# Kernel tuning notes

Hardware: AMD Instinct MI355X
Metric: run time of the kernel (lower is better)

The kernel has to match this reference:

```python
import jax, jax.numpy as jnp
import numpy as np

B, T, D, H, O = 64, 2048, 1024, 1024, 1024


def setup_inputs() -> dict:
    key = jax.random.key(0)
    ks = jax.random.split(key, 7)
    std = 1.0 / np.sqrt(H)
    u = lambda k, shape: jax.random.uniform(k, shape, jnp.float32, -std, std)
    return {
        "x": jax.random.normal(ks[0], (B, T, D), jnp.float32),
        "Wx": u(ks[1], (3 * H, D)),
        "bx": u(ks[2], (3 * H,)),
        "Wh": u(ks[3], (3 * H, H)),
        "bh": u(ks[4], (3 * H,)),
        "Wf": u(ks[5], (O, H)),
        "bf": u(ks[6], (O,)),
    }


def _gru_forward(x, Wx, bx, Wh, bh, Wf, bf):
    # Precompute input projections for all timesteps: [B, T, 3H]
    x_proj = jnp.einsum('btd,gd->btg', x, Wx) + bx

    def step(h, xp_t):
        # xp_t: [B, 3H], h: [B, H]
        h_proj = h @ Wh.T + bh
        x_r, x_u, x_n = jnp.split(xp_t, 3, axis=1)
        h_r, h_u, h_n = jnp.split(h_proj, 3, axis=1)
        reset = jax.nn.sigmoid(x_r + h_r)
        update = jax.nn.sigmoid(x_u + h_u)
        new = jnp.tanh(x_n + reset * h_n)
        hy = update * h + (1.0 - update) * new
        return hy, None

    h0 = jnp.zeros((x.shape[0], Wh.shape[1]), x.dtype)
    h_last, _ = jax.lax.scan(step, h0, jnp.swapaxes(x_proj, 0, 1))
    logits = h_last @ Wf.T + bf
    return jax.nn.log_softmax(logits, axis=-1)


def reference(x, Wx, bx, Wh, bh, Wf, bf):
    return _gru_forward(x, Wx, bx, Wh, bh, Wf, bf)
```

## Files before the change

kernel.cpp:

```cpp
#include <hip/hip_runtime.h>
#include <hip/hip_bf16.h>


#define Bb 64
#define Tt 2048
#define Dd 1024
#define Hh 1024

typedef __attribute__((ext_vector_type(8))) short bf16x8;
typedef __attribute__((ext_vector_type(4))) float f32x4;
typedef __attribute__((ext_vector_type(4))) unsigned int u32x4;

__device__ __forceinline__ short f2bf(float x) {
    __hip_bfloat16 h = __float2bfloat16(x);
    return __builtin_bit_cast(short, h);
}
__device__ __forceinline__ float bf2f(unsigned short u) {
    return __builtin_bit_cast(float, (unsigned)u << 16);
}
__device__ __forceinline__ bf16x8 pack8(float4 a, float4 b) {
    bf16x8 f;
    f[0] = f2bf(a.x); f[1] = f2bf(a.y); f[2] = f2bf(a.z); f[3] = f2bf(a.w);
    f[4] = f2bf(b.x); f[5] = f2bf(b.y); f[6] = f2bf(b.z); f[7] = f2bf(b.w);
    return f;
}
__device__ __forceinline__ unsigned long long ald64(const void* p) {
    return __hip_atomic_load((const unsigned long long*)p, __ATOMIC_RELAXED,
                             __HIP_MEMORY_SCOPE_AGENT);
}
__device__ __forceinline__ unsigned aldu32(const unsigned* p) {
    return __hip_atomic_load(p, __ATOMIC_RELAXED, __HIP_MEMORY_SCOPE_AGENT);
}

__global__ void wcvt(const float* __restrict__ a, unsigned short* __restrict__ o, long n) {
    long i = ((long)blockIdx.x * blockDim.x + threadIdx.x) * 8;
    long stride = (long)gridDim.x * blockDim.x * 8;
    for (; i < n; i += stride)
        *(bf16x8*)(o + i) = pack8(*(const float4*)(a + i), *(const float4*)(a + i + 4));
}

__global__ __launch_bounds__(256)
void xp_gemm(const float* __restrict__ x, const unsigned short* __restrict__ Wxb,
             unsigned short* __restrict__ xp, int t0) {
    __shared__ unsigned short As[64][40];
    const int tid = threadIdx.x;
    const int wave = tid >> 6, l = tid & 63, lm = l & 15, lk = l >> 4;
    const int slot = blockIdx.y;
    const int t = t0 + slot;
    const int n0w = blockIdx.x * 128 + wave * 32;

    f32x4 acc[4][2] = {};
#pragma unroll 1
    for (int k0 = 0; k0 < 1024; k0 += 32) {
        __syncthreads();
        {
            const int r = tid >> 2, kq = (tid & 3) * 8;
            const float* p = x + (size_t)r * Tt * Dd + (size_t)t * Dd + k0 + kq;
            *(bf16x8*)&As[r][kq] = pack8(*(const float4*)p, *(const float4*)(p + 4));
        }
        __syncthreads();
        bf16x8 bfr[2];
#pragma unroll
        for (int nt = 0; nt < 2; ++nt)
            bfr[nt] = *(const bf16x8*)(Wxb + (size_t)(n0w + nt * 16 + lm) * 1024 + k0 + lk * 8);
#pragma unroll
        for (int mt = 0; mt < 4; ++mt) {
            const bf16x8 af = *(const bf16x8*)&As[mt * 16 + lm][lk * 8];
            acc[mt][0] = __builtin_amdgcn_mfma_f32_16x16x32_bf16(af, bfr[0], acc[mt][0], 0, 0, 0);
            acc[mt][1] = __builtin_amdgcn_mfma_f32_16x16x32_bf16(af, bfr[1], acc[mt][1], 0, 0, 0);
        }
    }
#pragma unroll
    for (int mt = 0; mt < 4; ++mt)
#pragma unroll
        for (int nt = 0; nt < 2; ++nt)
#pragma unroll
            for (int i = 0; i < 4; ++i) {
                const int b = mt * 16 + lk * 4 + i;
                const int n = n0w + nt * 16 + lm;
                xp[((size_t)slot * 64 + b) * 3072 + n] = (unsigned short)f2bf(acc[mt][nt][i]);
            }
}

__global__ __launch_bounds__(512, 2)
void gru_scan8(const float* __restrict__ Wh, const float* __restrict__ bx,
               const float* __restrict__ bh, unsigned short* __restrict__ hl2,
               unsigned short* __restrict__ hmall,
               float* __restrict__ hstate, float* __restrict__ hfinal,
               const unsigned short* __restrict__ xp, unsigned* __restrict__ reg,
               int t0, int tend) {
    const int tid = threadIdx.x;
    const int w = tid >> 6, l = tid & 63, lm = l & 15, lk = l >> 4;

    __shared__ float comb[8][32][100];
    __shared__ float bxv[96], bhv[96];
    __shared__ unsigned s_gc;

    if (tid == 0) {
        unsigned xcc;
        asm volatile("s_getreg_b32 %0, hwreg(HW_REG_XCC_ID)" : "=s"(xcc));
        xcc &= 7u;
        unsigned r = __hip_atomic_fetch_add(&reg[xcc], 1u, __ATOMIC_RELAXED,
                                            __HIP_MEMORY_SCOPE_AGENT);
        __hip_atomic_fetch_add(&reg[8], 1u, __ATOMIC_RELEASE, __HIP_MEMORY_SCOPE_AGENT);
        while (__hip_atomic_load(&reg[8], __ATOMIC_ACQUIRE, __HIP_MEMORY_SCOPE_AGENT) < 256u)
            __builtin_amdgcn_s_sleep(8);
        bool bal = (r < 32u);
        for (int i = 0; i < 8; ++i)
            bal = bal && (__hip_atomic_load(&reg[i], __ATOMIC_RELAXED,
                                            __HIP_MEMORY_SCOPE_AGENT) == 32u);
        const unsigned g = bal ? xcc : (blockIdx.x & 7u);
        const unsigned c = bal ? r : (blockIdx.x >> 3);
        s_gc = (g << 8) | c;
    }
    __syncthreads();
    const int g = (s_gc >> 8) & 7, c = s_gc & 255;
    const int bg0 = g * 8, j0 = c * 32;
    const int kb = w * 128;

    if (tid < 96) {
        const int g3 = tid >> 5, jj = tid & 31;
        bxv[tid] = bx[g3 * 1024 + j0 + jj];
        bhv[tid] = bh[g3 * 1024 + j0 + jj];
    }
    const int grow = tid >> 4, jp = (tid & 15) * 2;
    float hp0 = 0.f, hp1 = 0.f;
    if (tid < 128) {
        const float2 h2 = *(const float2*)(hstate + (size_t)(bg0 + grow) * 1024 + j0 + jp);
        hp0 = h2.x; hp1 = h2.y;
    }

    bf16x8 wf[6][4];
#pragma unroll
    for (int nt = 0; nt < 6; ++nt) {
        const int n96 = nt * 16 + lm, g3 = n96 >> 5, jj = n96 & 31;
        const float* rp = Wh + (size_t)(g3 * 1024 + j0 + jj) * 1024 + kb + lk * 8;
#pragma unroll
        for (int ks = 0; ks < 4; ++ks)
            wf[nt][ks] = pack8(*(const float4*)(rp + ks * 32), *(const float4*)(rp + ks * 32 + 4));
    }
    __syncthreads();

    unsigned xa0 = 0, xa1 = 0, xa2 = 0, xb0 = 0, xb1 = 0, xb2 = 0;
    if (tid < 128) {
        const unsigned short* xr = xp + ((size_t)0 * 64 + bg0 + grow) * 3072 + j0 + jp;
        xa0 = *(const unsigned*)(xr);
        xa1 = *(const unsigned*)(xr + 1024);
        xa2 = *(const unsigned*)(xr + 2048);
    }

    const int row_a = (lm < 8) ? lm : 7;
    u32x4 f0, f1, f2, f3;
    int useMall = 0;

#define L2LOAD4(P)                                                             \
    asm volatile(                                                              \
        "global_load_dwordx4 %[r0], %[ad], off sc0\n\t"                        \
        "global_load_dwordx4 %[r1], %[ad], off offset:64 sc0\n\t"              \
        "global_load_dwordx4 %[r2], %[ad], off offset:128 sc0\n\t"             \
        "global_load_dwordx4 %[r3], %[ad], off offset:192 sc0\n\t"             \
        "s_waitcnt vmcnt(0)"                                                   \
        : [r0] "=&v"(f0), [r1] "=&v"(f1), [r2] "=&v"(f2), [r3] "=&v"(f3)       \
        : [ad] "v"(P)                                                          \
        : "memory")
#define MLOAD4(P)                                                              \
    do {                                                                       \
        struct UU { unsigned long long a, b; };                                \
        UU u0{ald64(P), ald64((P) + 4)};                                       \
        UU u1{ald64((P) + 32), ald64((P) + 36)};                               \
        UU u2{ald64((P) + 64), ald64((P) + 68)};                               \
        UU u3{ald64((P) + 96), ald64((P) + 100)};                              \
        f0 = __builtin_bit_cast(u32x4, u0);                                    \
        f1 = __builtin_bit_cast(u32x4, u1);                                    \
        f2 = __builtin_bit_cast(u32x4, u2);                                    \
        f3 = __builtin_bit_cast(u32x4, u3);                                    \
    } while (0)
#define TAG4(F) (((F)[0] ^ tg) | ((F)[1] ^ tg) | ((F)[2] ^ tg) | ((F)[3] ^ tg))

#pragma unroll 1
    for (int t = t0; t < tend; ++t) {
        const size_t hoff = (size_t)(t & 1) * 65536 + (size_t)g * 8192
                            + (size_t)row_a * 1024 + kb + lk * 8;
        const unsigned tg = (unsigned)(t >> 1) & 1u;

        if (!useMall) {
            const unsigned short* pl = hl2 + hoff;
            int spins = 0;
            for (;;) {
                L2LOAD4(pl);
                const unsigned bad = (TAG4(f0) | TAG4(f1) | TAG4(f2) | TAG4(f3)) & 1u;
                if (__builtin_expect(__all((int)(bad == 0u)), 1)) break;
                if (++spins > 512) { useMall = 1; break; }
            }
        }
        if (useMall) {
            const unsigned short* pm = hmall + hoff;
            for (;;) {
                MLOAD4(pm);
                const unsigned bad = (TAG4(f0) | TAG4(f1) | TAG4(f2) | TAG4(f3)) & 1u;
                if (__builtin_expect(__all((int)(bad == 0u)), 1)) break;
                __builtin_amdgcn_s_sleep(1);
            }
        }

        if (tid < 128 && t + 1 < tend) {
            const unsigned short* xr = xp + ((size_t)(t + 1 - t0) * 64 + bg0 + grow) * 3072 + j0 + jp;
            xb0 = *(const unsigned*)(xr);
            xb1 = *(const unsigned*)(xr + 1024);
            xb2 = *(const unsigned*)(xr + 2048);
        }

        f32x4 acc[6] = {};
#define KSTEP(F, KS)                                                            \
        do {                                                                    \
            const bf16x8 af = __builtin_bit_cast(bf16x8, F);                    \
            _Pragma("unroll")                                                   \
            for (int nt = 0; nt < 6; ++nt)                                      \
                acc[nt] = __builtin_amdgcn_mfma_f32_16x16x32_bf16(              \
                    af, wf[nt][KS], acc[nt], 0, 0, 0);                          \
        } while (0)
        KSTEP(f0, 0); KSTEP(f1, 1); KSTEP(f2, 2); KSTEP(f3, 3);
#undef KSTEP

        if (lk < 2) {
#pragma unroll
            for (int nt = 0; nt < 6; ++nt)
#pragma unroll
                for (int i = 0; i < 4; ++i)
                    comb[w][lk * 4 + i][nt * 16 + lm] = acc[nt][i];
        }
        asm volatile("s_waitcnt lgkmcnt(0)\ns_barrier" ::: "memory");

        if (tid < 128) {
            float s00 = 0, s10 = 0, s20 = 0, s01 = 0, s11 = 0, s21 = 0;
#pragma unroll
            for (int ww = 0; ww < 8; ++ww) {
                s00 += comb[ww][grow][jp];      s01 += comb[ww][grow][jp + 1];
                s10 += comb[ww][grow][32 + jp]; s11 += comb[ww][grow][33 + jp];
                s20 += comb[ww][grow][64 + jp]; s21 += comb[ww][grow][65 + jp];
            }
            const float xr0 = bf2f((unsigned short)xa0) + bxv[jp];
            const float xr1 = bf2f((unsigned short)(xa0 >> 16)) + bxv[jp + 1];
            const float xu0 = bf2f((unsigned short)xa1) + bxv[32 + jp];
            const float xu1 = bf2f((unsigned short)(xa1 >> 16)) + bxv[33 + jp];
            const float xn0 = bf2f((unsigned short)xa2) + bxv[64 + jp];
            const float xn1 = bf2f((unsigned short)(xa2 >> 16)) + bxv[65 + jp];
            const float r0 = 1.0f / (1.0f + __expf(-(xr0 + s00 + bhv[jp])));
            const float r1 = 1.0f / (1.0f + __expf(-(xr1 + s01 + bhv[jp + 1])));
            const float u0 = 1.0f / (1.0f + __expf(-(xu0 + s10 + bhv[32 + jp])));
            const float u1 = 1.0f / (1.0f + __expf(-(xu1 + s11 + bhv[33 + jp])));
            const float z0 = xn0 + r0 * (s20 + bhv[64 + jp]);
            const float z1 = xn1 + r1 * (s21 + bhv[65 + jp]);
            const float e0 = __expf(2.0f * z0), e1 = __expf(2.0f * z1);
            const float n0 = 1.0f - 2.0f / (e0 + 1.0f);
            const float n1 = 1.0f - 2.0f / (e1 + 1.0f);
            const float hy0 = u0 * hp0 + (1.0f - u0) * n0;
            const float hy1 = u1 * hp1 + (1.0f - u1) * n1;
            hp0 = hy0; hp1 = hy1;
            const unsigned tagn = ((unsigned)(t + 1) >> 1) & 1u;
            const unsigned v0 = ((unsigned)(unsigned short)f2bf(hy0) & 0xFFFEu) | tagn;
            const unsigned pk = ((unsigned)(unsigned short)f2bf(hy1) << 16) | v0;
            const size_t soff = (size_t)((t + 1) & 1) * 65536 + (size_t)g * 8192
                                + (size_t)grow * 1024 + j0 + jp;
            *(volatile unsigned*)(hl2 + soff) = pk;
            __hip_atomic_store((unsigned*)(hmall + soff), pk, __ATOMIC_RELAXED,
                               __HIP_MEMORY_SCOPE_AGENT);
            if (t == tend - 1)
                *(float2*)(hstate + (size_t)(bg0 + grow) * 1024 + j0 + jp) = make_float2(hy0, hy1);
            if (t == Tt - 1)
                *(float2*)(hfinal + (size_t)(bg0 + grow) * 1024 + j0 + jp) = make_float2(hy0, hy1);
            xa0 = xb0; xa1 = xb1; xa2 = xb2;
        }
        asm volatile("s_barrier" ::: "memory");
    }
#undef L2LOAD4
#undef MLOAD4
#undef TAG4
}

template <bool RING>
__global__ __launch_bounds__(256, 1)
void gru_scan(const float* __restrict__ x,
              const float* __restrict__ Wx, const float* __restrict__ bx,
              const float* __restrict__ Wh, const float* __restrict__ bh,
              unsigned short* __restrict__ hbuf, float* __restrict__ hfinal,
              unsigned short* __restrict__ ring, unsigned* __restrict__ flags) {
    const int tid = threadIdx.x;
    const int w   = tid >> 6;
    const int l   = tid & 63;
    const int bid = blockIdx.x;
    const int g   = bid & 1;
    const int c   = bid >> 1;
    const int bg0 = g * 32;
    const int j0  = c * 8;

    __shared__ float comb[4][32][24];
    __shared__ float hp[32][8];
    __shared__ float bxv[24], bhv[24];

    hp[tid >> 3][tid & 7] = 0.0f;
    if (tid < 24) {
        const int gate = tid >> 3, jj = tid & 7;
        bxv[tid] = bx[gate * 1024 + j0 + jj];
        bhv[tid] = bh[gate * 1024 + j0 + jj];
    }

    const int lm = l & 15;
    const int lk = l >> 4;
    const int wb = w * 512;
    bf16x8 bfr[2][16];
    {
        const float* Wbase = (w < 2) ? Wx : Wh;
        const int krel = (w < 2) ? wb : (wb - 1024);
#pragma unroll
        for (int nt = 0; nt < 2; ++nt) {
            int row24 = nt * 16 + lm;
            if (row24 > 23) row24 = 23;
            const int gate = row24 >> 3, jj = row24 & 7;
            const float* rp = Wbase + (size_t)(gate * 1024 + j0 + jj) * 1024 + krel + lk * 8;
#pragma unroll
            for (int ks = 0; ks < 16; ++ks) {
                float4 a = *(const float4*)(rp + ks * 32);
                float4 b = *(const float4*)(rp + ks * 32 + 4);
                bfr[nt][ks] = pack8(a, b);
            }
        }
    }
    __syncthreads();

    if (RING) {
        if (tid < 128) {
            const int e = c * 256 + tid * 2;
            const int rl = e >> 10, col = e & 1023;
#pragma unroll
            for (int s = 0; s < 4; ++s) {
                const float2 xv = *(const float2*)(x + ((size_t)(bg0 + rl) * Tt + s) * Dd + col);
                unsigned pk = (unsigned)(unsigned short)f2bf(xv.x)
                            | ((unsigned)(unsigned short)f2bf(xv.y) << 16);
                __hip_atomic_store((unsigned*)(ring + (size_t)s * 65536
                                               + (size_t)(bg0 + rl) * 1024 + col),
                                   pk, __ATOMIC_RELAXED, __HIP_MEMORY_SCOPE_AGENT);
            }
        }
        asm volatile("s_waitcnt vmcnt(0)" ::: "memory");
        __syncthreads();
        if (tid == 0)
            __hip_atomic_store(&flags[g * 128 + c], 1u, __ATOMIC_RELAXED,
                               __HIP_MEMORY_SCOPE_AGENT);
        if (tid < 128) {
            const unsigned* f = flags + g * 128 + tid;
            while (aldu32(f) < 1u) __builtin_amdgcn_s_sleep(1);
        }
        asm volatile("" ::: "memory");
        __syncthreads();
    }

#pragma unroll 1
    for (int t = 0; t < Tt; ++t) {
        const unsigned short* hcur = hbuf + (size_t)(t & 1) * Bb * Hh;

        if (RING && tid < 128) {
            const int sp = t + 4;
            if (sp < Tt) {
                const int e = c * 256 + tid * 2;
                const int rl = e >> 10, col = e & 1023;
                const float2 xv = *(const float2*)(x + ((size_t)(bg0 + rl) * Tt + sp) * Dd + col);
                unsigned pk = (unsigned)(unsigned short)f2bf(xv.x)
                            | ((unsigned)(unsigned short)f2bf(xv.y) << 16);
                __hip_atomic_store((unsigned*)(ring + (size_t)(sp & 7) * 65536
                                               + (size_t)(bg0 + rl) * 1024 + col),
                                   pk, __ATOMIC_RELAXED, __HIP_MEMORY_SCOPE_AGENT);
            }
        }

        if (w >= 2 && t > 0) {
            const unsigned tgt = (unsigned)(t + 1);
            const unsigned* f0 = flags + g * 128 + l;
            const unsigned* f1 = f0 + 64;
            while (aldu32(f0) < tgt || aldu32(f1) < tgt) __builtin_amdgcn_s_sleep(1);
        }
        asm volatile("" ::: "memory");

        f32x4 acc[2][2] = {};
        if (RING || w >= 2) {
            const unsigned short* src;
            int colb;
            if (w < 2) { src = ring + (size_t)(t & 7) * 65536; colb = wb; }
            else       { src = hcur;                           colb = wb - 1024; }
#pragma unroll
            for (int half = 0; half < 2; ++half) {
                unsigned long long stg[8][2][2];
#pragma unroll
                for (int k8 = 0; k8 < 8; ++k8) {
                    const int ks = half * 8 + k8;
#pragma unroll
                    for (int mt = 0; mt < 2; ++mt) {
                        const unsigned short* p = src + (size_t)(bg0 + mt * 16 + lm) * 1024
                                                  + colb + ks * 32 + lk * 8;
                        stg[k8][mt][0] = ald64(p);
                        stg[k8][mt][1] = ald64(p + 4);
                    }
                }
#pragma unroll
                for (int k8 = 0; k8 < 8; ++k8) {
                    const int ks = half * 8 + k8;
#pragma unroll
                    for (int mt = 0; mt < 2; ++mt) {
                        struct { unsigned long long a, b; } u{stg[k8][mt][0], stg[k8][mt][1]};
                        bf16x8 af = __builtin_bit_cast(bf16x8, u);
                        acc[mt][0] = __builtin_amdgcn_mfma_f32_16x16x32_bf16(af, bfr[0][ks], acc[mt][0], 0, 0, 0);
                        acc[mt][1] = __builtin_amdgcn_mfma_f32_16x16x32_bf16(af, bfr[1][ks], acc[mt][1], 0, 0, 0);
                    }
                }
            }
        } else {
#pragma unroll
            for (int ks = 0; ks < 16; ++ks) {
#pragma unroll
                for (int mt = 0; mt < 2; ++mt) {
                    const size_t row = (size_t)(bg0 + mt * 16 + lm);
                    const size_t off = (row * Tt + t) * Dd + wb + ks * 32 + lk * 8;
                    float4 a = *(const float4*)(x + off);
                    float4 b = *(const float4*)(x + off + 4);
                    bf16x8 af = pack8(a, b);
                    acc[mt][0] = __builtin_amdgcn_mfma_f32_16x16x32_bf16(af, bfr[0][ks], acc[mt][0], 0, 0, 0);
                    acc[mt][1] = __builtin_amdgcn_mfma_f32_16x16x32_bf16(af, bfr[1][ks], acc[mt][1], 0, 0, 0);
                }
            }
        }

#pragma unroll
        for (int mt = 0; mt < 2; ++mt)
#pragma unroll
            for (int nt = 0; nt < 2; ++nt) {
                const int n = nt * 16 + lm;
                if (n < 24) {
#pragma unroll
                    for (int i = 0; i < 4; ++i)
                        comb[w][mt * 16 + lk * 4 + i][n] = acc[mt][nt][i];
                }
            }
        __syncthreads();

        {
            const int b = tid >> 3, j = tid & 7;
            const float rz = comb[0][b][j] + comb[1][b][j] + comb[2][b][j] + comb[3][b][j]
                             + bxv[j] + bhv[j];
            const float uz = comb[0][b][8 + j] + comb[1][b][8 + j] + comb[2][b][8 + j]
                             + comb[3][b][8 + j] + bxv[8 + j] + bhv[8 + j];
            const float nx = comb[0][b][16 + j] + comb[1][b][16 + j] + bxv[16 + j];
            const float nh = comb[2][b][16 + j] + comb[3][b][16 + j] + bhv[16 + j];
            const float r  = 1.0f / (1.0f + __expf(-rz));
            const float u  = 1.0f / (1.0f + __expf(-uz));
            const float zz = nx + r * nh;
            const float e2 = __expf(2.0f * zz);
            const float nv = 1.0f - 2.0f / (e2 + 1.0f);
            const float hold = hp[b][j];
            const float hy = u * hold + (1.0f - u) * nv;
            hp[b][j] = hy;
            unsigned short* hn = hbuf + (size_t)((t + 1) & 1) * Bb * Hh
                                 + (size_t)(bg0 + b) * 1024 + j0 + j;
            __hip_atomic_store(hn, (unsigned short)f2bf(hy), __ATOMIC_RELAXED,
                               __HIP_MEMORY_SCOPE_AGENT);
            if (t == Tt - 1) hfinal[(size_t)(bg0 + b) * 1024 + j0 + j] = hy;
        }
        asm volatile("s_waitcnt vmcnt(0)" ::: "memory");
        __syncthreads();
        if (tid == 0 && t + 1 < Tt)
            __hip_atomic_store(&flags[g * 128 + c], (unsigned)(t + 2), __ATOMIC_RELAXED,
                               __HIP_MEMORY_SCOPE_AGENT);
    }
}

__global__ __launch_bounds__(1024)
void final_kernel(const float* __restrict__ hfinal, const float* __restrict__ Wf,
                  const float* __restrict__ bfv, float* __restrict__ out) {
    const int b = blockIdx.x;
    const int o = threadIdx.x;
    __shared__ float hs[1024];
    __shared__ float redm[16], redsum[16], bcast[2];
    hs[o] = hfinal[(size_t)b * 1024 + o];
    __syncthreads();

    const float* wr = Wf + (size_t)o * 1024;
    float acc = bfv[o];
#pragma unroll 4
    for (int k = 0; k < 1024; k += 4) {
        float4 wv = *(const float4*)(wr + k);
        acc += hs[k] * wv.x + hs[k + 1] * wv.y + hs[k + 2] * wv.z + hs[k + 3] * wv.w;
    }

    float m = acc;
#pragma unroll
    for (int off = 32; off > 0; off >>= 1) m = fmaxf(m, __shfl_xor(m, off));
    if ((o & 63) == 0) redm[o >> 6] = m;
    __syncthreads();
    if (o == 0) {
        float mm = redm[0];
#pragma unroll
        for (int i = 1; i < 16; ++i) mm = fmaxf(mm, redm[i]);
        bcast[0] = mm;
    }
    __syncthreads();
    const float bm = bcast[0];
    float s = __expf(acc - bm);
#pragma unroll
    for (int off = 32; off > 0; off >>= 1) s += __shfl_xor(s, off);
    if ((o & 63) == 0) redsum[o >> 6] = s;
    __syncthreads();
    if (o == 0) {
        float ss = 0.0f;
        for (int i = 0; i < 16; ++i) ss += redsum[i];
        bcast[1] = logf(ss);
    }
    __syncthreads();
    out[(size_t)b * 1024 + o] = acc - bm - bcast[1];
}

extern "C" void kernel_launch(void* const* d_in, const int* in_sizes, int n_in,
                              void* d_out, int out_size, void* d_ws, size_t ws_size,
                              hipStream_t stream) {
    (void)in_sizes; (void)n_in; (void)out_size;
    const float* x   = (const float*)d_in[0];
    const float* Wx  = (const float*)d_in[1];
    const float* bx  = (const float*)d_in[2];
    const float* Wh  = (const float*)d_in[3];
    const float* bh  = (const float*)d_in[4];
    const float* Wf  = (const float*)d_in[5];
    const float* bfv = (const float*)d_in[6];
    float* out = (float*)d_out;
    char* ws = (char*)d_ws;

    const size_t RG = 0;
    const size_t HL = 4096;
    const size_t HM = HL + 262144;
    const size_t HS = HM + 262144;
    const size_t HF = HS + 262144;
    const size_t WX = HF + 262144;
    const size_t XP = WX + 6291456;
    size_t avail = (ws_size > XP) ? (ws_size - XP) : 0;
    long Wl = (long)(avail / 393216);
    if (Wl > 2048) Wl = 2048;
    const int W = (int)Wl;

    if (W >= 32) {
        unsigned* reg         = (unsigned*)(ws + RG);
        unsigned short* hl2   = (unsigned short*)(ws + HL);
        unsigned short* hmall = (unsigned short*)(ws + HM);
        float* hstate         = (float*)(ws + HS);
        float* hfinal         = (float*)(ws + HF);
        unsigned short* Wxb   = (unsigned short*)(ws + WX);
        unsigned short* xp    = (unsigned short*)(ws + XP);

        hipMemsetAsync(ws + RG, 0x00, 4096, stream);
        hipMemsetAsync(ws + HL, 0x00, 131072, stream);
        hipMemsetAsync(ws + HL + 131072, 0xFF, 131072, stream);
        hipMemsetAsync(ws + HM, 0x00, 131072, stream);
        hipMemsetAsync(ws + HM + 131072, 0xFF, 131072, stream);
        hipMemsetAsync(ws + HS, 0x00, 262144, stream);
        wcvt<<<1536, 256, 0, stream>>>(Wx, (unsigned short*)Wxb, 3L * 1024 * 1024);
        int chunk = 0;
        for (int t0 = 0; t0 < Tt; t0 += W, ++chunk) {
            const int Wc = (Tt - t0 < W) ? (Tt - t0) : W;
            xp_gemm<<<dim3(24, Wc), 256, 0, stream>>>(x, Wxb, xp, t0);
            gru_scan8<<<256, 512, 0, stream>>>(Wh, bx, bh, hl2, hmall, hstate,
                                               hfinal, xp, reg + chunk * 16,
                                               t0, t0 + Wc);
        }
        final_kernel<<<64, 1024, 0, stream>>>(hfinal, Wf, bfv, out);
    } else {
        unsigned* flags      = (unsigned*)ws;
        unsigned short* hbuf = (unsigned short*)(ws + 1024);
        float* hfinal        = (float*)(ws + 1024 + 262144);
        unsigned short* ring = (unsigned short*)(ws + 1024 + 262144 + 262144);
        const size_t need_ring = 1024 + 262144 + 262144 + (size_t)8 * 131072;
        const bool use_ring = (ws_size >= need_ring);

        hipMemsetAsync(d_ws, 0, 1024 + (size_t)Bb * Hh * 2, stream);
        if (use_ring)
            gru_scan<true><<<256, 256, 0, stream>>>(x, Wx, bx, Wh, bh, hbuf, hfinal, ring, flags);
        else
            gru_scan<false><<<256, 256, 0, stream>>>(x, Wx, bx, Wh, bh, hbuf, hfinal, ring, flags);
        final_kernel<<<64, 1024, 0, stream>>>(hfinal, Wf, bfv, out);
    }
}
```

Measured before the change: 10.38 ms.

## Double-buffer reduction scratch, drop trailing barrier and XCC-aware block placement

Makes the per-step cross-wave reduction buffer double-buffered by timestep parity, which lets the second barrier at the end of each step be removed. It also removes the XCC-based block-to-tile assignment (atomic registration and spin) and uses a plain blockIdx mapping, and drops the sleep in the MALL polling loop. The aim is lower per-step synchronisation latency on the recurrence's critical path. In exchange, blocks sharing a batch group may land on different XCDs, so L2-local h exchange happens less often and the slower MALL fallback may be used more.

```diff
diff --git a/kernel.cpp b/kernel.cpp
--- a/kernel.cpp
+++ b/kernel.cpp
@@ -83,40 +83,20 @@
 }
 
 __global__ __launch_bounds__(512, 2)
-void gru_scan8(const float* __restrict__ Wh, const float* __restrict__ bx,
+void gru_scanA(const float* __restrict__ Wh, const float* __restrict__ bx,
                const float* __restrict__ bh, unsigned short* __restrict__ hl2,
                unsigned short* __restrict__ hmall,
                float* __restrict__ hstate, float* __restrict__ hfinal,
-               const unsigned short* __restrict__ xp, unsigned* __restrict__ reg,
-               int t0, int tend) {
+               const unsigned short* __restrict__ xp, int t0, int tend) {
     const int tid = threadIdx.x;
     const int w = tid >> 6, l = tid & 63, lm = l & 15, lk = l >> 4;
-
-    __shared__ float comb[8][32][100];
-    __shared__ float bxv[96], bhv[96];
-    __shared__ unsigned s_gc;
-
-    if (tid == 0) {
-        unsigned xcc;
-        asm volatile("s_getreg_b32 %0, hwreg(HW_REG_XCC_ID)" : "=s"(xcc));
-        xcc &= 7u;
-        unsigned r = __hip_atomic_fetch_add(&reg[xcc], 1u, __ATOMIC_RELAXED,
-                                            __HIP_MEMORY_SCOPE_AGENT);
-        __hip_atomic_fetch_add(&reg[8], 1u, __ATOMIC_RELEASE, __HIP_MEMORY_SCOPE_AGENT);
-        while (__hip_atomic_load(&reg[8], __ATOMIC_ACQUIRE, __HIP_MEMORY_SCOPE_AGENT) < 256u)
-            __builtin_amdgcn_s_sleep(8);
-        bool bal = (r < 32u);
-        for (int i = 0; i < 8; ++i)
-            bal = bal && (__hip_atomic_load(&reg[i], __ATOMIC_RELAXED,
-                                            __HIP_MEMORY_SCOPE_AGENT) == 32u);
-        const unsigned g = bal ? xcc : (blockIdx.x & 7u);
-        const unsigned c = bal ? r : (blockIdx.x >> 3);
-        s_gc = (g << 8) | c;
-    }
-    __syncthreads();
-    const int g = (s_gc >> 8) & 7, c = s_gc & 255;
+    const int bid = blockIdx.x;
+    const int g = bid & 7, c = bid >> 3;
     const int bg0 = g * 8, j0 = c * 32;
     const int kb = w * 128;
+
+    __shared__ float comb[2][8][16][100];
+    __shared__ float bxv[96], bhv[96];
 
     if (tid < 96) {
         const int g3 = tid >> 5, jj = tid & 31;
@@ -199,7 +179,6 @@
                 MLOAD4(pm);
                 const unsigned bad = (TAG4(f0) | TAG4(f1) | TAG4(f2) | TAG4(f3)) & 1u;
                 if (__builtin_expect(__all((int)(bad == 0u)), 1)) break;
-                __builtin_amdgcn_s_sleep(1);
             }
         }
 
@@ -227,7 +206,7 @@
             for (int nt = 0; nt < 6; ++nt)
 #pragma unroll
                 for (int i = 0; i < 4; ++i)
-                    comb[w][lk * 4 + i][nt * 16 + lm] = acc[nt][i];
+                    comb[t & 1][w][lk * 4 + i][nt * 16 + lm] = acc[nt][i];
         }
         asm volatile("s_waitcnt lgkmcnt(0)\ns_barrier" ::: "memory");
 
@@ -235,9 +214,9 @@
             float s00 = 0, s10 = 0, s20 = 0, s01 = 0, s11 = 0, s21 = 0;
 #pragma unroll
             for (int ww = 0; ww < 8; ++ww) {
-                s00 += comb[ww][grow][jp];      s01 += comb[ww][grow][jp + 1];
-                s10 += comb[ww][grow][32 + jp]; s11 += comb[ww][grow][33 + jp];
-                s20 += comb[ww][grow][64 + jp]; s21 += comb[ww][grow][65 + jp];
+                s00 += comb[t & 1][ww][grow][jp];      s01 += comb[t & 1][ww][grow][jp + 1];
+                s10 += comb[t & 1][ww][grow][32 + jp]; s11 += comb[t & 1][ww][grow][33 + jp];
+                s20 += comb[t & 1][ww][grow][64 + jp]; s21 += comb[t & 1][ww][grow][65 + jp];
             }
             const float xr0 = bf2f((unsigned short)xa0) + bxv[jp];
             const float xr1 = bf2f((unsigned short)(xa0 >> 16)) + bxv[jp + 1];
@@ -271,7 +250,6 @@
                 *(float2*)(hfinal + (size_t)(bg0 + grow) * 1024 + j0 + jp) = make_float2(hy0, hy1);
             xa0 = xb0; xa1 = xb1; xa2 = xb2;
         }
-        asm volatile("s_barrier" ::: "memory");
     }
 #undef L2LOAD4
 #undef MLOAD4
@@ -531,8 +509,7 @@
     float* out = (float*)d_out;
     char* ws = (char*)d_ws;
 
-    const size_t RG = 0;
-    const size_t HL = 4096;
+    const size_t HL = 1024;
     const size_t HM = HL + 262144;
     const size_t HS = HM + 262144;
     const size_t HF = HS + 262144;
@@ -544,7 +521,6 @@
     const int W = (int)Wl;
 
     if (W >= 32) {
-        unsigned* reg         = (unsigned*)(ws + RG);
         unsigned short* hl2   = (unsigned short*)(ws + HL);
         unsigned short* hmall = (unsigned short*)(ws + HM);
         float* hstate         = (float*)(ws + HS);
@@ -552,20 +528,17 @@
         unsigned short* Wxb   = (unsigned short*)(ws + WX);
         unsigned short* xp    = (unsigned short*)(ws + XP);
 
-        hipMemsetAsync(ws + RG, 0x00, 4096, stream);
         hipMemsetAsync(ws + HL, 0x00, 131072, stream);
         hipMemsetAsync(ws + HL + 131072, 0xFF, 131072, stream);
         hipMemsetAsync(ws + HM, 0x00, 131072, stream);
         hipMemsetAsync(ws + HM + 131072, 0xFF, 131072, stream);
         hipMemsetAsync(ws + HS, 0x00, 262144, stream);
         wcvt<<<1536, 256, 0, stream>>>(Wx, (unsigned short*)Wxb, 3L * 1024 * 1024);
-        int chunk = 0;
-        for (int t0 = 0; t0 < Tt; t0 += W, ++chunk) {
+        for (int t0 = 0; t0 < Tt; t0 += W) {
             const int Wc = (Tt - t0 < W) ? (Tt - t0) : W;
             xp_gemm<<<dim3(24, Wc), 256, 0, stream>>>(x, Wxb, xp, t0);
-            gru_scan8<<<256, 512, 0, stream>>>(Wh, bx, bh, hl2, hmall, hstate,
-                                               hfinal, xp, reg + chunk * 16,
-                                               t0, t0 + Wc);
+            gru_scanA<<<256, 512, 0, stream>>>(Wh, bx, bh, hl2, hmall, hstate,
+                                               hfinal, xp, t0, t0 + Wc);
         }
         final_kernel<<<64, 1024, 0, stream>>>(hfinal, Wf, bfv, out);
     } else {
```

Result: slower. 13.48 ms (+29.8%).
